# Performance work log

Measured on AMD Instinct MI355X. Metric: run time of the kernel, lower is better.

## Reference

```python
import jax, jax.numpy as jnp
import numpy as np

DIM = 768
HEADS = 12
HEAD_DIM = DIM // HEADS
SCALE = HEAD_DIM ** (-0.5)


def setup_inputs() -> dict:
    key = jax.random.key(0)
    k1, k2, k3 = jax.random.split(key, 3)
    x = jax.random.normal(k1, (4, 2048, DIM), dtype=jnp.float32)
    # nn.Linear(dim, 3*dim, bias=False): weight [3*dim, dim]
    w_qkv = jax.random.normal(k2, (3 * DIM, DIM), dtype=jnp.float32) * (DIM ** -0.5)
    # nn.Linear(dim, dim) with bias
    w_proj = jax.random.normal(k3, (DIM, DIM), dtype=jnp.float32) * (DIM ** -0.5)
    b_proj = jnp.zeros((DIM,), dtype=jnp.float32)
    return {"x": x, "w_qkv": w_qkv, "w_proj": w_proj, "b_proj": b_proj}


def reference(x, w_qkv, w_proj, b_proj):
    B, N, C = x.shape
    H, D = HEADS, HEAD_DIM
    qkv = jnp.einsum('bnc,oc->bno', x, w_qkv)  # [B,N,3C]
    qkv = qkv.reshape(B, N, 3, H, D).transpose(2, 0, 3, 1, 4)  # [3,B,H,N,D]
    q, k, v = qkv[0], qkv[1], qkv[2]
    attn = jnp.einsum('bhnd,bhmd->bhnm', q, k) * SCALE  # [B,H,N,N]
    attn = jax.nn.softmax(attn, axis=-1)
    attn = jax.nn.softmax(attn, axis=-1)  # double softmax, as in original
    out = jnp.einsum('bhnm,bhmd->bhnd', attn, v)  # [B,H,N,D]
    out = out.transpose(0, 2, 1, 3).reshape(B, N, C)
    return jnp.einsum('bnc,oc->bno', out, w_proj) + b_proj
```

## Files before the change

### kernel.cpp

```cpp
#include <hip/hip_runtime.h>
#include <hip/hip_bf16.h>

#define DIM 768
#define HEADS 12
#define HD 64
#define SEQ 2048
#define BATCH 4
#define BHN 48
#define TOK 8192

#if __has_builtin(__builtin_amdgcn_exp2f)
#define EXP2F __builtin_amdgcn_exp2f
#else
#define EXP2F exp2f
#endif
#define EXP_C 0.1803368801111244f

using short8  = __attribute__((ext_vector_type(8))) short;
using short4v = __attribute__((ext_vector_type(4))) short;
using float4v = __attribute__((ext_vector_type(4))) float;

__device__ __forceinline__ short f2b(float f) {
    union { float f; unsigned u; } v; v.f = f;
    unsigned r = v.u + 0x7FFF + ((v.u >> 16) & 1);
    return (short)(r >> 16);
}
__device__ __forceinline__ float b2f(short s) {
    union { unsigned u; float f; } v;
    v.u = ((unsigned)(unsigned short)s) << 16;
    return v.f;
}
__device__ __forceinline__ unsigned pk2(float a, float b) {
    union { float f; unsigned u; } x, y; x.f = a; y.f = b;
    return ((x.u + 0x8000u) >> 16) | ((y.u + 0x8000u) & 0xFFFF0000u);
}

typedef const __attribute__((address_space(1))) unsigned GU;
typedef __attribute__((address_space(3))) unsigned LU;
__device__ __forceinline__ void gload_lds16(const short* g, short* l) {
    __builtin_amdgcn_global_load_lds((GU*)g, (LU*)l, 16, 0, 0);
}

__global__ void cast_all(const float* __restrict__ x, const float* __restrict__ wq,
                         const float* __restrict__ wp,
                         short* __restrict__ xb, short* __restrict__ wqb,
                         short* __restrict__ wpb, int nx4, int nq4) {
    int i = blockIdx.x * 256 + threadIdx.x;
    const float* in; short* out; int j = i;
    if (i < nx4)            { in = x;  out = xb;  }
    else if (i < nx4 + nq4) { in = wq; out = wqb; j = i - nx4; }
    else                    { in = wp; out = wpb; j = i - nx4 - nq4; }
    float4 f = ((const float4*)in)[j];
    short4 o;
    o.x = f2b(f.x); o.y = f2b(f.y); o.z = f2b(f.z); o.w = f2b(f.w);
    ((short4*)out)[j] = o;
}

__global__ void vsum_kernel(const short* __restrict__ Vw, float* __restrict__ Vsum) {
    int wid  = blockIdx.x * 4 + (threadIdx.x >> 6);
    int lane = threadIdx.x & 63;
    const short* row = Vw + (size_t)wid * SEQ;
    float s = 0.f;
    for (int i = lane; i < SEQ; i += 64) s += b2f(row[i]);
    #pragma unroll
    for (int m = 1; m < 64; m <<= 1) s += __shfl_xor(s, m, 64);
    if (lane == 0) Vsum[wid] = s;
}

__global__ __launch_bounds__(256, 4)
void gemm_qkv(const short* __restrict__ A, const short* __restrict__ Bw,
              short* __restrict__ Qw, short* __restrict__ Kw, short* __restrict__ Vw)
{
    __shared__ __align__(16) short As[2][128 * 32];
    __shared__ __align__(16) short Bs[2][128 * 32];

    const int tid  = threadIdx.x;
    const int lane = tid & 63;
    const int wave = tid >> 6;
    const int wm = (wave >> 1) * 64, wn = (wave & 1) * 64;
    const int l15 = lane & 15, quad = lane >> 4;

    const int gid = blockIdx.x;
    const int w   = gid >> 3;
    const int ybl = (gid & 7) * 8 + (w & 7);
    const int xbl = w >> 3;

    const bool vpart = (xbl >= 12);
    const short* rowsP = vpart ? (Bw + 1536 * 768) : A;
    const short* colsP = vpart ? A : Bw;
    const int m0 = vpart ? (xbl - 12) * 128 : ybl * 128;
    const int n0 = vpart ? ybl * 128 : xbl * 128;
    const int K = DIM;

    float4v acc[4][4];
    #pragma unroll
    for (int i = 0; i < 4; i++)
        #pragma unroll
        for (int j = 0; j < 4; j++)
            acc[i][j] = (float4v){0.f, 0.f, 0.f, 0.f};

    const int G0 = wave * 128 + lane;
    const int G1 = G0 + 64;
    const int rA0 = G0 >> 2, cA0 = (G0 & 3) * 8;
    const int rA1 = G1 >> 2, cA1 = (G1 & 3) * 8;
    const int ldsoff = wave * 1024;

    for (int kt = 0; kt < K; kt += 64) {
        #pragma unroll
        for (int s = 0; s < 2; s++) {
            const int kc = kt + s * 32;
            gload_lds16(&rowsP[(size_t)(m0 + rA0) * K + kc + cA0], &As[s][ldsoff]);
            gload_lds16(&rowsP[(size_t)(m0 + rA1) * K + kc + cA1], &As[s][ldsoff + 512]);
            gload_lds16(&colsP[(size_t)(n0 + rA0) * K + kc + cA0], &Bs[s][ldsoff]);
            gload_lds16(&colsP[(size_t)(n0 + rA1) * K + kc + cA1], &Bs[s][ldsoff + 512]);
        }
        __syncthreads();
        #pragma unroll
        for (int s = 0; s < 2; s++) {
            short8 af[4], bfr[4];
            #pragma unroll
            for (int t = 0; t < 4; t++) {
                af[t]  = *(const short8*)&As[s][(wm + t * 16 + l15) * 32 + quad * 8];
                bfr[t] = *(const short8*)&Bs[s][(wn + t * 16 + l15) * 32 + quad * 8];
            }
            #pragma unroll
            for (int tm = 0; tm < 4; tm++)
                #pragma unroll
                for (int tn = 0; tn < 4; tn++)
                    acc[tm][tn] = __builtin_amdgcn_mfma_f32_16x16x32_bf16(af[tm], bfr[tn], acc[tm][tn], 0, 0, 0);
        }
        __syncthreads();
    }

    #pragma unroll
    for (int tm = 0; tm < 4; tm++)
        #pragma unroll
        for (int tn = 0; tn < 4; tn++)
            #pragma unroll
            for (int r = 0; r < 4; r++) {
                int row = m0 + wm + tm * 16 + quad * 4 + r;
                int col = n0 + wn + tn * 16 + l15;
                float v = acc[tm][tn][r];
                if (vpart) {
                    int hh = row >> 6, d = row & 63;
                    int b = col >> 11, n = col & 2047;
                    Vw[((size_t)(b * HEADS + hh) * 64 + d) * SEQ + n] = f2b(v);
                } else {
                    int hh = (col & 767) >> 6, d = col & 63;
                    int b = row >> 11, n = row & 2047;
                    int bh = b * HEADS + hh;
                    if (col < 768) Qw[((size_t)bh * SEQ + n) * 64 + d] = f2b(v * EXP_C);
                    else           Kw[((size_t)bh * SEQ + n) * 64 + d] = f2b(v);
                }
            }
}

__global__ __launch_bounds__(256, 4)
void gemm_proj(const short* __restrict__ A, const short* __restrict__ Bw,
               const float* __restrict__ bias, float* __restrict__ Out)
{
    __shared__ __align__(16) short As[2][128 * 32];
    __shared__ __align__(16) short Bs[2][64 * 32];

    const int tid  = threadIdx.x;
    const int lane = tid & 63;
    const int wave = tid >> 6;
    const int wm = (wave >> 1) * 64, wn = (wave & 1) * 32;
    const int l15 = lane & 15, quad = lane >> 4;

    const int gid = blockIdx.x;
    const int w   = gid >> 3;
    const int ybl = (gid & 7) * 8 + (w & 7);
    const int xbl = w >> 3;
    const int m0 = ybl * 128, n0 = xbl * 64;
    const int K = DIM;

    float4v acc[4][2];
    #pragma unroll
    for (int i = 0; i < 4; i++)
        #pragma unroll
        for (int j = 0; j < 2; j++)
            acc[i][j] = (float4v){0.f, 0.f, 0.f, 0.f};

    const int GA0 = wave * 128 + lane, GA1 = GA0 + 64;
    const int rA0 = GA0 >> 2, cA0 = (GA0 & 3) * 8;
    const int rA1 = GA1 >> 2, cA1 = (GA1 & 3) * 8;
    const int GB0 = wave * 64 + lane;
    const int rB0 = GB0 >> 2, cB0 = (GB0 & 3) * 8;
    const int ldsoffA = wave * 1024, ldsoffB = wave * 512;

    for (int kt = 0; kt < K; kt += 64) {
        #pragma unroll
        for (int s = 0; s < 2; s++) {
            const int kc = kt + s * 32;
            gload_lds16(&A [(size_t)(m0 + rA0) * K + kc + cA0], &As[s][ldsoffA]);
            gload_lds16(&A [(size_t)(m0 + rA1) * K + kc + cA1], &As[s][ldsoffA + 512]);
            gload_lds16(&Bw[(size_t)(n0 + rB0) * K + kc + cB0], &Bs[s][ldsoffB]);
        }
        __syncthreads();
        #pragma unroll
        for (int s = 0; s < 2; s++) {
            short8 af[4], bfr[2];
            #pragma unroll
            for (int t = 0; t < 4; t++)
                af[t] = *(const short8*)&As[s][(wm + t * 16 + l15) * 32 + quad * 8];
            #pragma unroll
            for (int t = 0; t < 2; t++)
                bfr[t] = *(const short8*)&Bs[s][(wn + t * 16 + l15) * 32 + quad * 8];
            #pragma unroll
            for (int tm = 0; tm < 4; tm++)
                #pragma unroll
                for (int tn = 0; tn < 2; tn++)
                    acc[tm][tn] = __builtin_amdgcn_mfma_f32_16x16x32_bf16(af[tm], bfr[tn], acc[tm][tn], 0, 0, 0);
        }
        __syncthreads();
    }

    #pragma unroll
    for (int tm = 0; tm < 4; tm++)
        #pragma unroll
        for (int tn = 0; tn < 2; tn++)
            #pragma unroll
            for (int r = 0; r < 4; r++) {
                int row = m0 + wm + tm * 16 + quad * 4 + r;
                int col = n0 + wn + tn * 16 + l15;
                Out[(size_t)row * 768 + col] = acc[tm][tn][r] + bias[col];
            }
}

__global__ __launch_bounds__(256, 4)
void attn_kernel(const short* __restrict__ Qw, const short* __restrict__ Kw,
                 const short* __restrict__ Vw, const float* __restrict__ Vsum,
                 short* __restrict__ Ow)
{
    __shared__ __align__(16) short KE[128 * 72];
    __shared__ __align__(16) short Vt[64 * 136];

    const int tid  = threadIdx.x;
    const int lane = tid & 63, wave = tid >> 6;
    const int l15 = lane & 15, quad = lane >> 4;
    const int bh = blockIdx.x >> 5;
    const int n0 = (blockIdx.x & 31) * 64;
    const int wq = (wave & 2) * 16;
    const int wk = (wave & 1) * 64;

    const short* Qp = Qw + (size_t)bh * SEQ * 64;
    const short* Kp = Kw + (size_t)bh * SEQ * 64;
    const short* Vp = Vw + (size_t)bh * 64 * SEQ;

    short8 onesf;
    #pragma unroll
    for (int j = 0; j < 8; j++) onesf[j] = (l15 == 0) ? (short)0x3F80 : (short)0;

    #pragma unroll
    for (int h = 0; h < 2; h++) {
        int c = tid + h * 256;
        int row = c >> 3, cc = (c & 7) * 8;
        *(short8*)&KE[row * 72 + cc] = *(const short8*)&Qp[(size_t)(n0 + row) * 64 + cc];
    }
    __syncthreads();
    short8 aq[2][2];
    #pragma unroll
    for (int nb = 0; nb < 2; nb++)
        #pragma unroll
        for (int kk = 0; kk < 2; kk++)
            aq[nb][kk] = *(const short8*)&KE[(wq + nb * 16 + l15) * 72 + kk * 32 + quad * 8];

    float4v Aacc[2][4], Lacc[2];
    #pragma unroll
    for (int mb = 0; mb < 2; mb++) {
        Lacc[mb] = (float4v){0.f, 0.f, 0.f, 0.f};
        #pragma unroll
        for (int t = 0; t < 4; t++) Aacc[mb][t] = (float4v){0.f, 0.f, 0.f, 0.f};
    }

    const int svc   = ((tid & 15) * 8);
    const int svrow = tid >> 4;
    const int sw0   = svc & 31;
    const int svp1  = (svc & 96) + (((sw0 & 8) << 1) | ((sw0 & 16) >> 2));

    short8 kr[4], vr[4];
    #pragma unroll
    for (int h = 0; h < 4; h++) {
        int c = tid + h * 256;
        int row = c >> 3, cc = (c & 7) * 8;
        kr[h] = *(const short8*)&Kp[(size_t)row * 64 + cc];
        int vrow = c >> 4, vc = (c & 15) * 8;
        vr[h] = *(const short8*)&Vp[(size_t)vrow * SEQ + vc];
    }

    for (int kt = 0; kt < 16; kt++) {
        __syncthreads();
        #pragma unroll
        for (int h = 0; h < 4; h++) {
            int c = tid + h * 256;
            int row = c >> 3, cc = (c & 7) * 8;
            *(short8*)&KE[row * 72 + cc] = kr[h];
            int vrow = svrow + h * 16;
            short4v lo = __builtin_shufflevector(vr[h], vr[h], 0, 1, 2, 3);
            short4v hi = __builtin_shufflevector(vr[h], vr[h], 4, 5, 6, 7);
            *(short4v*)&Vt[vrow * 136 + svp1]     = lo;
            *(short4v*)&Vt[vrow * 136 + svp1 + 8] = hi;
        }
        __syncthreads();

        if (kt < 15) {
            #pragma unroll
            for (int h = 0; h < 4; h++) {
                int c = tid + h * 256;
                int row = c >> 3, cc = (c & 7) * 8;
                kr[h] = *(const short8*)&Kp[(size_t)((kt + 1) * 128 + row) * 64 + cc];
                int vrow = c >> 4, vc = (c & 15) * 8;
                vr[h] = *(const short8*)&Vp[(size_t)vrow * SEQ + (kt + 1) * 128 + vc];
            }
        }

        union AE { unsigned u[4]; short8 s; };
        AE ae[2][2];
        #pragma unroll
        for (int tn = 0; tn < 4; tn++) {
            const int rowK = (wk + tn * 16 + l15) * 72;
            short8 b0 = *(const short8*)&KE[rowK + quad * 8];
            short8 b1 = *(const short8*)&KE[rowK + 32 + quad * 8];
            #pragma unroll
            for (int nb = 0; nb < 2; nb++) {
                float4v s = (float4v){0.f, 0.f, 0.f, 0.f};
                s = __builtin_amdgcn_mfma_f32_16x16x32_bf16(b0, aq[nb][0], s, 0, 0, 0);
                s = __builtin_amdgcn_mfma_f32_16x16x32_bf16(b1, aq[nb][1], s, 0, 0, 0);
                ae[nb][tn >> 1].u[(tn & 1) * 2]     = pk2(EXP2F(s[0]), EXP2F(s[1]));
                ae[nb][tn >> 1].u[(tn & 1) * 2 + 1] = pk2(EXP2F(s[2]), EXP2F(s[3]));
            }
        }

        #pragma unroll
        for (int c2 = 0; c2 < 2; c2++) {
            Lacc[0] = __builtin_amdgcn_mfma_f32_16x16x32_bf16(ae[0][c2].s, onesf, Lacc[0], 0, 0, 0);
            Lacc[1] = __builtin_amdgcn_mfma_f32_16x16x32_bf16(ae[1][c2].s, onesf, Lacc[1], 0, 0, 0);
            #pragma unroll
            for (int tn = 0; tn < 4; tn++) {
                short8 bv = *(const short8*)&Vt[(tn * 16 + l15) * 136 + wk + c2 * 32 + quad * 8];
                Aacc[0][tn] = __builtin_amdgcn_mfma_f32_16x16x32_bf16(ae[0][c2].s, bv, Aacc[0][tn], 0, 0, 0);
                Aacc[1][tn] = __builtin_amdgcn_mfma_f32_16x16x32_bf16(ae[1][c2].s, bv, Aacc[1][tn], 0, 0, 0);
            }
        }
    }

    __syncthreads();
    float* KEf = (float*)KE;
    float* Vtf = (float*)Vt;
    const int p = wave >> 1;
    if (wave & 1) {
        #pragma unroll
        for (int mb = 0; mb < 2; mb++) {
            #pragma unroll
            for (int tn = 0; tn < 4; tn++)
                #pragma unroll
                for (int r = 0; r < 4; r++)
                    KEf[(mb * 16 + tn * 4 + r) * 128 + p * 64 + lane] = Aacc[mb][tn][r];
            #pragma unroll
            for (int r = 0; r < 4; r++)
                Vtf[(mb * 4 + r) * 128 + p * 64 + lane] = Lacc[mb][r];
        }
    }
    __syncthreads();
    if (!(wave & 1)) {
        float il[2][4];
        #pragma unroll
        for (int mb = 0; mb < 2; mb++)
            #pragma unroll
            for (int r = 0; r < 4; r++) {
                float ls = Lacc[mb][r] + Vtf[(mb * 4 + r) * 128 + p * 64 + lane];
                il[mb][r] = 1.f / __shfl(ls, lane & 48, 64);
            }
        const int b = bh / HEADS, hh = bh - (bh / HEADS) * HEADS;
        #pragma unroll
        for (int tn = 0; tn < 4; tn++) {
            int d = tn * 16 + l15;
            float vs = Vsum[bh * 64 + d];
            #pragma unroll
            for (int mb = 0; mb < 2; mb++)
                #pragma unroll
                for (int r = 0; r < 4; r++) {
                    float a = Aacc[mb][tn][r] + KEf[(mb * 16 + tn * 4 + r) * 128 + p * 64 + lane];
                    int row = n0 + wq + mb * 16 + quad * 4 + r;
                    float val = (vs + a * il[mb][r]) * (1.f / 2049.f);
                    int tok = b * SEQ + row;
                    Ow[(size_t)tok * 768 + hh * 64 + d] = f2b(val);
                }
        }
    }
}

extern "C" void kernel_launch(void* const* d_in, const int* in_sizes, int n_in,
                              void* d_out, int out_size, void* d_ws, size_t ws_size,
                              hipStream_t stream) {
    const float* x      = (const float*)d_in[0];
    const float* w_qkv  = (const float*)d_in[1];
    const float* w_proj = (const float*)d_in[2];
    const float* b_proj = (const float*)d_in[3];
    float* out = (float*)d_out;

    char* ws = (char*)d_ws;
    size_t off = 0;
    auto alloc = [&](size_t bytes) {
        void* p = ws + off;
        off += (bytes + 255) & ~(size_t)255;
        return p;
    };
    short* x_bf  = (short*)alloc((size_t)TOK * DIM * 2);
    short* wq_bf = (short*)alloc((size_t)3 * DIM * DIM * 2);
    short* wp_bf = (short*)alloc((size_t)DIM * DIM * 2);
    short* Qw    = (short*)alloc((size_t)BHN * SEQ * 64 * 2);
    short* Kw    = (short*)alloc((size_t)BHN * SEQ * 64 * 2);
    short* Vw    = (short*)alloc((size_t)BHN * SEQ * 64 * 2);
    short* Ow    = (short*)alloc((size_t)TOK * DIM * 2);
    float* Vsum  = (float*)alloc((size_t)BHN * 64 * 4);

    int nx4 = TOK * DIM / 4, nq4 = 3 * DIM * DIM / 4, np4 = DIM * DIM / 4;
    int tot4 = nx4 + nq4 + np4;
    cast_all<<<tot4 / 256, 256, 0, stream>>>(x, w_qkv, w_proj, x_bf, wq_bf, wp_bf, nx4, nq4);

    gemm_qkv<<<1152, 256, 0, stream>>>(x_bf, wq_bf, Qw, Kw, Vw);

    vsum_kernel<<<BHN * 64 / 4, 256, 0, stream>>>(Vw, Vsum);

    attn_kernel<<<BHN * 32, 256, 0, stream>>>(Qw, Kw, Vw, Vsum, Ow);

    gemm_proj<<<768, 256, 0, stream>>>(Ow, wp_bf, b_proj, out);
}
```

Baseline: 219.9 us.

## Give each attention wave full key tiles over 128 queries, drop cross-wave reduction

```diff
diff --git a/kernel.cpp b/kernel.cpp
--- a/kernel.cpp
+++ b/kernel.cpp
@@ -32,7 +32,7 @@
 }
 __device__ __forceinline__ unsigned pk2(float a, float b) {
     union { float f; unsigned u; } x, y; x.f = a; y.f = b;
-    return ((x.u + 0x8000u) >> 16) | ((y.u + 0x8000u) & 0xFFFF0000u);
+    return __builtin_amdgcn_perm(x.u + 0x8000u, y.u + 0x8000u, 0x03020706u);
 }
 
 typedef const __attribute__((address_space(1))) unsigned GU;
@@ -228,7 +228,7 @@
             }
 }
 
-__global__ __launch_bounds__(256, 4)
+__global__ __launch_bounds__(256, 3)
 void attn_kernel(const short* __restrict__ Qw, const short* __restrict__ Kw,
                  const short* __restrict__ Vw, const float* __restrict__ Vsum,
                  short* __restrict__ Ow)
@@ -239,10 +239,9 @@
     const int tid  = threadIdx.x;
     const int lane = tid & 63, wave = tid >> 6;
     const int l15 = lane & 15, quad = lane >> 4;
-    const int bh = blockIdx.x >> 5;
-    const int n0 = (blockIdx.x & 31) * 64;
-    const int wq = (wave & 2) * 16;
-    const int wk = (wave & 1) * 64;
+    const int bh = blockIdx.x >> 4;
+    const int n0 = (blockIdx.x & 15) * 128;
+    const int wq = wave * 32;
 
     const short* Qp = Qw + (size_t)bh * SEQ * 64;
     const short* Kp = Kw + (size_t)bh * SEQ * 64;
@@ -253,7 +252,7 @@
     for (int j = 0; j < 8; j++) onesf[j] = (l15 == 0) ? (short)0x3F80 : (short)0;
 
     #pragma unroll
-    for (int h = 0; h < 2; h++) {
+    for (int h = 0; h < 4; h++) {
         int c = tid + h * 256;
         int row = c >> 3, cc = (c & 7) * 8;
         *(short8*)&KE[row * 72 + cc] = *(const short8*)&Qp[(size_t)(n0 + row) * 64 + cc];
@@ -315,80 +314,54 @@
             }
         }
 
-        union AE { unsigned u[4]; short8 s; };
-        AE ae[2][2];
-        #pragma unroll
-        for (int tn = 0; tn < 4; tn++) {
-            const int rowK = (wk + tn * 16 + l15) * 72;
-            short8 b0 = *(const short8*)&KE[rowK + quad * 8];
-            short8 b1 = *(const short8*)&KE[rowK + 32 + quad * 8];
-            #pragma unroll
-            for (int nb = 0; nb < 2; nb++) {
-                float4v s = (float4v){0.f, 0.f, 0.f, 0.f};
-                s = __builtin_amdgcn_mfma_f32_16x16x32_bf16(b0, aq[nb][0], s, 0, 0, 0);
-                s = __builtin_amdgcn_mfma_f32_16x16x32_bf16(b1, aq[nb][1], s, 0, 0, 0);
-                ae[nb][tn >> 1].u[(tn & 1) * 2]     = pk2(EXP2F(s[0]), EXP2F(s[1]));
-                ae[nb][tn >> 1].u[(tn & 1) * 2 + 1] = pk2(EXP2F(s[2]), EXP2F(s[3]));
-            }
-        }
-
-        #pragma unroll
-        for (int c2 = 0; c2 < 2; c2++) {
-            Lacc[0] = __builtin_amdgcn_mfma_f32_16x16x32_bf16(ae[0][c2].s, onesf, Lacc[0], 0, 0, 0);
-            Lacc[1] = __builtin_amdgcn_mfma_f32_16x16x32_bf16(ae[1][c2].s, onesf, Lacc[1], 0, 0, 0);
+        #pragma unroll
+        for (int c2 = 0; c2 < 4; c2++) {
+            union AE { unsigned u[4]; short8 s; };
+            AE ae[2];
+            #pragma unroll
+            for (int tn2 = 0; tn2 < 2; tn2++) {
+                const int tn = c2 * 2 + tn2;
+                const int rowK = (tn * 16 + l15) * 72;
+                short8 b0 = *(const short8*)&KE[rowK + quad * 8];
+                short8 b1 = *(const short8*)&KE[rowK + 32 + quad * 8];
+                #pragma unroll
+                for (int nb = 0; nb < 2; nb++) {
+                    float4v s = (float4v){0.f, 0.f, 0.f, 0.f};
+                    s = __builtin_amdgcn_mfma_f32_16x16x32_bf16(b0, aq[nb][0], s, 0, 0, 0);
+                    s = __builtin_amdgcn_mfma_f32_16x16x32_bf16(b1, aq[nb][1], s, 0, 0, 0);
+                    ae[nb].u[tn2 * 2]     = pk2(EXP2F(s[0]), EXP2F(s[1]));
+                    ae[nb].u[tn2 * 2 + 1] = pk2(EXP2F(s[2]), EXP2F(s[3]));
+                }
+            }
+            __builtin_amdgcn_s_setprio(1);
+            Lacc[0] = __builtin_amdgcn_mfma_f32_16x16x32_bf16(ae[0].s, onesf, Lacc[0], 0, 0, 0);
+            Lacc[1] = __builtin_amdgcn_mfma_f32_16x16x32_bf16(ae[1].s, onesf, Lacc[1], 0, 0, 0);
             #pragma unroll
             for (int tn = 0; tn < 4; tn++) {
-                short8 bv = *(const short8*)&Vt[(tn * 16 + l15) * 136 + wk + c2 * 32 + quad * 8];
-                Aacc[0][tn] = __builtin_amdgcn_mfma_f32_16x16x32_bf16(ae[0][c2].s, bv, Aacc[0][tn], 0, 0, 0);
-                Aacc[1][tn] = __builtin_amdgcn_mfma_f32_16x16x32_bf16(ae[1][c2].s, bv, Aacc[1][tn], 0, 0, 0);
-            }
-        }
-    }
-
-    __syncthreads();
-    float* KEf = (float*)KE;
-    float* Vtf = (float*)Vt;
-    const int p = wave >> 1;
-    if (wave & 1) {
-        #pragma unroll
-        for (int mb = 0; mb < 2; mb++) {
-            #pragma unroll
-            for (int tn = 0; tn < 4; tn++)
-                #pragma unroll
-                for (int r = 0; r < 4; r++)
-                    KEf[(mb * 16 + tn * 4 + r) * 128 + p * 64 + lane] = Aacc[mb][tn][r];
-            #pragma unroll
-            for (int r = 0; r < 4; r++)
-                Vtf[(mb * 4 + r) * 128 + p * 64 + lane] = Lacc[mb][r];
-        }
-    }
-    __syncthreads();
-    if (!(wave & 1)) {
-        float il[2][4];
-        #pragma unroll
-        for (int mb = 0; mb < 2; mb++)
-            #pragma unroll
-            for (int r = 0; r < 4; r++) {
-                float ls = Lacc[mb][r] + Vtf[(mb * 4 + r) * 128 + p * 64 + lane];
-                il[mb][r] = 1.f / __shfl(ls, lane & 48, 64);
-            }
-        const int b = bh / HEADS, hh = bh - (bh / HEADS) * HEADS;
-        #pragma unroll
-        for (int tn = 0; tn < 4; tn++) {
-            int d = tn * 16 + l15;
-            float vs = Vsum[bh * 64 + d];
-            #pragma unroll
-            for (int mb = 0; mb < 2; mb++)
-                #pragma unroll
-                for (int r = 0; r < 4; r++) {
-                    float a = Aacc[mb][tn][r] + KEf[(mb * 16 + tn * 4 + r) * 128 + p * 64 + lane];
-                    int row = n0 + wq + mb * 16 + quad * 4 + r;
-                    float val = (vs + a * il[mb][r]) * (1.f / 2049.f);
-                    int tok = b * SEQ + row;
-                    Ow[(size_t)tok * 768 + hh * 64 + d] = f2b(val);
-                }
-        }
-    }
+                short8 bv = *(const short8*)&Vt[(tn * 16 + l15) * 136 + c2 * 32 + quad * 8];
+                Aacc[0][tn] = __builtin_amdgcn_mfma_f32_16x16x32_bf16(ae[0].s, bv, Aacc[0][tn], 0, 0, 0);
+                Aacc[1][tn] = __builtin_amdgcn_mfma_f32_16x16x32_bf16(ae[1].s, bv, Aacc[1][tn], 0, 0, 0);
+            }
+            __builtin_amdgcn_s_setprio(0);
+        }
+    }
+
+    const int b = bh / HEADS, hh = bh - (bh / HEADS) * HEADS;
+    #pragma unroll
+    for (int mb = 0; mb < 2; mb++)
+        #pragma unroll
+        for (int r = 0; r < 4; r++) {
+            float il = 1.f / __shfl(Lacc[mb][r], lane & 48, 64);
+            int row = n0 + wq + mb * 16 + quad * 4 + r;
+            int tok = b * SEQ + row;
+            #pragma unroll
+            for (int tn = 0; tn < 4; tn++) {
+                int d = tn * 16 + l15;
+                float vs = Vsum[bh * 64 + d];
+                float val = (vs + Aacc[mb][tn][r] * il) * (1.f / 2049.f);
+                Ow[(size_t)tok * 768 + hh * 64 + d] = f2b(val);
+            }
+        }
 }
 
 extern "C" void kernel_launch(void* const* d_in, const int* in_sizes, int n_in,
@@ -424,7 +397,7 @@
 
     vsum_kernel<<<BHN * 64 / 4, 256, 0, stream>>>(Vw, Vsum);
 
-    attn_kernel<<<BHN * 32, 256, 0, stream>>>(Qw, Kw, Vw, Vsum, Ow);
+    attn_kernel<<<BHN * 16, 256, 0, stream>>>(Qw, Kw, Vw, Vsum, Ow);
 
     gemm_proj<<<768, 256, 0, stream>>>(Ow, wp_bf, b_proj, out);
 }
```

Measured after the change: 209.3 us. 1.05x faster.
